# Kernel tuning notes

Hardware: AMD Instinct MI355X
Metric: run time of the kernel (lower is better)

Reference implementation:

```python
import jax, jax.numpy as jnp
import numpy as np
import math

N, IFZ, NVZ, AHZ, QPZ, KZ, PEZ = 1024, 256, 64, 8, 4, 20, 20
NUM_FREQ = PEZ // 2
FREQ_INV = 50.0

def layer_norm(x, g, b, eps=1e-5):
    mu = x.mean(-1, keepdims=True)
    var = ((x - mu) ** 2).mean(-1, keepdims=True)
    return (x - mu) / jnp.sqrt(var + eps) * g + b

def setup_inputs() -> dict:
    key = jax.random.key(0)
    ks = jax.random.split(key, 8)
    x = jax.random.normal(ks[0], (N, IFZ), jnp.float32)
    affines = jax.random.normal(ks[1], (N, 3, 4), jnp.float32)
    prot_mask = jnp.ones((N,), dtype=bool)
    edge_index = jax.random.randint(ks[2], (N, KZ), 0, N, dtype=jnp.int32)
    s = 0.02
    w_nde = jax.random.normal(ks[3], (KZ * 3 * PEZ, NVZ), jnp.float32) * s
    b_nde = jnp.zeros((NVZ,), jnp.float32)
    w_q = jax.random.normal(ks[4], (IFZ + NVZ, AHZ * QPZ * 3), jnp.float32) * s
    w_v = jax.random.normal(ks[5], (IFZ + NVZ, AHZ * QPZ * IFZ), jnp.float32) * s
    ln_ag_g = jnp.ones((AHZ * QPZ * IFZ,), jnp.float32)
    ln_ag_b = jnp.zeros((AHZ * QPZ * IFZ,), jnp.float32)
    w_ag = jax.random.normal(ks[6], (AHZ * QPZ * IFZ, IFZ), jnp.float32) * s
    ln_en_g = jnp.ones((IFZ,), jnp.float32)
    ln_en_b = jnp.zeros((IFZ,), jnp.float32)
    return dict(x=x, affines=affines, prot_mask=prot_mask, edge_index=edge_index,
                w_nde=w_nde, b_nde=b_nde, w_q=w_q, w_v=w_v,
                ln_ag_g=ln_ag_g, ln_ag_b=ln_ag_b, w_ag=w_ag,
                ln_en_g=ln_en_g, ln_en_b=ln_en_b)

def reference(x, affines, prot_mask, edge_index, w_nde, b_nde, w_q, w_v,
              ln_ag_g, ln_ag_b, w_ag, ln_en_g, ln_en_b):
    dtype = x.dtype
    R = affines[:, :, :3]                                   # (N,3,3) rotation
    t = affines[:, :, 3]                                    # (N,3) translation
    positions = t
    # --- BackboneDistanceEmbedding (reconstructed): local neighbour vectors ---
    rel = positions[edge_index] - t[:, None, :]             # (N,K,3)
    local = jnp.einsum('nji,nkj->nki', R, rel)              # inverse-affine (R^T) (N,K,3)
    freqs = jnp.arange(1, NUM_FREQ + 1, dtype=dtype) / FREQ_INV
    ang = local[..., None] * freqs                          # (N,K,3,F)
    pe = jnp.concatenate([jnp.sin(ang), jnp.cos(ang)], -1)  # (N,K,3,PEZ)
    nv = jax.nn.relu(pe.reshape(x.shape[0], -1) @ w_nde + b_nde)  # (N,NVZ)
    nv = nv * prot_mask[:, None].astype(dtype)
    x_ne = jnp.concatenate([x, nv], axis=-1)                # (N,IFZ+NVZ)
    # --- query points in global frame ---
    q = (x_ne @ w_q).reshape(-1, 1, AHZ, QPZ, 3)
    q = jnp.einsum('nij,nkaqj->nkaqi', R, q) + t[:, None, None, None, :]
    gnp = positions[edge_index][:, :, None, None, :]        # (N,K,1,1,3)
    # --- L2-distance attention over neighbourhood ---
    scores = -jnp.linalg.norm(q - gnp, axis=-1).sum(-1)     # (N,K,AHZ)
    attn = jax.nn.softmax(scores, axis=1).astype(dtype)
    # --- value gather + weighted aggregation ---
    v = (x_ne @ w_v).reshape(-1, AHZ, QPZ, IFZ)
    v_ne = v[edge_index]                                    # (N,K,AHZ,QPZ,IFZ) -- big gather
    new = jnp.einsum('nkaqi,nka->naqi', v_ne, attn).reshape(x.shape[0], -1)
    new = layer_norm(new, ln_ag_g, ln_ag_b) @ w_ag          # dropout: eval mode => identity
    out = layer_norm(x + new / math.sqrt(2.0), ln_en_g, ln_en_b).astype(dtype)
    return out, edge_index
```

## Files before the change

kernel.cpp:

```cpp
#include <hip/hip_runtime.h>
#include <hip/hip_bf16.h>
#include <math.h>

#define NNODE 1024
#define IFZ   256
#define NVZ   64
#define AHZ   8
#define QPZ   4
#define KZ    20
#define NF    10
#define XNE   320
#define VROW  8192
#define PEK   1280
#define PTOT  2560

typedef unsigned short ushort;
typedef __attribute__((ext_vector_type(8))) short    short8v;
typedef __attribute__((ext_vector_type(8))) ushort   ushort8v;
typedef __attribute__((ext_vector_type(4))) float    float4v;

static __device__ __forceinline__ ushort f2bf(float f) {
    unsigned u = __float_as_uint(f);
    unsigned r = 0x7FFFu + ((u >> 16) & 1u);
    return (ushort)((u + r) >> 16);
}
static __device__ __forceinline__ float bf2f(unsigned h) {
    return __uint_as_float(h << 16);
}

struct Params {
    const float *w_ag, *ln_ag_g, *ln_ag_b, *w_nde, *b_nde, *w_q, *w_v, *x, *aff;
    const int   *edge;
    const float *ln_en_g, *ln_en_b;
    ushort *wagT, *wndeT, *wqT, *wv_bf, *pebf, *xne_bf, *agg, *WcT, *G;
    float  *rsum, *vpart, *vconst, *qbuf, *geom, *S, *s2part, *tmpk, *out;
};

static __device__ __forceinline__ void gemm_tile(
    const ushort* __restrict__ A, const ushort* __restrict__ BT,
    int aStride, int btStride, int kLen, int bm, int bn, int tid,
    float4v acc[2][2], ushort (&As)[64][40], ushort (&Bs)[64][40])
{
    const int w = tid >> 6, lane = tid & 63;
    const int wr = w >> 1, wc = w & 1;
    const int lane15 = lane & 15, quad = lane >> 4;
    const int sm = tid >> 2, sk = (tid & 3) * 8;
    for (int k0 = 0; k0 < kLen; k0 += 32) {
        *(ushort8v*)&As[sm][sk] = *(const ushort8v*)&A[(size_t)(bm + sm)*aStride + k0 + sk];
        *(ushort8v*)&Bs[sm][sk] = *(const ushort8v*)&BT[(size_t)(bn + sm)*btStride + k0 + sk];
        __syncthreads();
        short8v a0 = *(const short8v*)&As[wr*32      + lane15][quad*8];
        short8v a1 = *(const short8v*)&As[wr*32 + 16 + lane15][quad*8];
        short8v b0 = *(const short8v*)&Bs[wc*32      + lane15][quad*8];
        short8v b1 = *(const short8v*)&Bs[wc*32 + 16 + lane15][quad*8];
        acc[0][0] = __builtin_amdgcn_mfma_f32_16x16x32_bf16(a0, b0, acc[0][0], 0, 0, 0);
        acc[0][1] = __builtin_amdgcn_mfma_f32_16x16x32_bf16(a0, b1, acc[0][1], 0, 0, 0);
        acc[1][0] = __builtin_amdgcn_mfma_f32_16x16x32_bf16(a1, b0, acc[1][0], 0, 0, 0);
        acc[1][1] = __builtin_amdgcn_mfma_f32_16x16x32_bf16(a1, b1, acc[1][1], 0, 0, 0);
        __syncthreads();
    }
}

#define T1_END 2048
#define T2_END 2128
#define T3_END 2168
#define CV_END 2488
#define GV_END 2552
#define K0_END 2808

__global__ __launch_bounds__(256) void k_prep(Params P)
{
    const int u = blockIdx.x;
    const int tid = threadIdx.x;
    __shared__ float t[32][33];
    __shared__ float part[256];
    __shared__ float tn[4][KZ][3];
    __shared__ float r9[4][9], tt[4][3];

    if (u < T3_END) {
        const float* src; ushort* dst; const float* scl;
        int R, C, gx, Rdst, rel;
        if (u < T1_END)      { src=P.w_ag; dst=P.wagT; scl=P.ln_ag_g; R=VROW; C=IFZ; gx=8; Rdst=VROW; rel=u; }
        else if (u < T2_END) { src=P.w_nde;dst=P.wndeT;scl=nullptr;   R=1200; C=NVZ; gx=2; Rdst=PEK;  rel=u-T1_END; }
        else                 { src=P.w_q;  dst=P.wqT;  scl=nullptr;   R=XNE;  C=96;  gx=4; Rdst=XNE;  rel=u-T2_END; }
        const int bx = rel % gx, by = rel / gx;
        const int c0 = bx*32, r0 = by*32;
        const int tx = tid & 31, ty = tid >> 5;
        #pragma unroll
        for (int i = 0; i < 4; ++i) {
            int r = r0 + ty + 8*i, c = c0 + tx;
            float v = (r < R && c < C) ? src[(size_t)r * C + c] : 0.f;
            if (scl && r < R) v *= scl[r];
            t[ty + 8*i][tx] = v;
        }
        __syncthreads();
        #pragma unroll
        for (int i = 0; i < 4; ++i)
            dst[(size_t)(c0 + ty + 8*i) * Rdst + r0 + tx] = f2bf(t[tx][ty + 8*i]);
    } else if (u < CV_END) {
        const int j = u - T3_END;
        const float* src = P.w_v + (size_t)j*VROW + tid*32;
        ushort* dst = P.wv_bf + (size_t)j*VROW + tid*32;
        float psum = 0.f;
        #pragma unroll
        for (int q = 0; q < 4; ++q) {
            float4 v0 = ((const float4*)src)[q*2];
            float4 v1 = ((const float4*)src)[q*2+1];
            psum += v0.x+v0.y+v0.z+v0.w + v1.x+v1.y+v1.z+v1.w;
            ushort8v o;
            o[0]=f2bf(v0.x); o[1]=f2bf(v0.y); o[2]=f2bf(v0.z); o[3]=f2bf(v0.w);
            o[4]=f2bf(v1.x); o[5]=f2bf(v1.y); o[6]=f2bf(v1.z); o[7]=f2bf(v1.w);
            *(ushort8v*)(dst + q*8) = o;
        }
        part[tid] = psum;
        __syncthreads();
        if (tid < 8) {
            float s = 0.f;
            #pragma unroll
            for (int v = 0; v < 32; ++v) s += part[tid*32 + v];
            P.rsum[tid*320 + j] = s;
        }
    } else if (u < GV_END) {
        const int sp = u - CV_END, j = tid;
        const float* base = P.w_ag + (size_t)sp * 128 * IFZ;
        float vp = 0.f, bp = 0.f;
        #pragma unroll 4
        for (int r = 0; r < 128; ++r) {
            float wv = base[(size_t)r * IFZ + j];
            vp += P.ln_ag_g[sp*128 + r] * wv;
            bp += P.ln_ag_b[sp*128 + r] * wv;
        }
        P.vpart[(size_t)(sp*2 + 0) * IFZ + j] = vp;
        P.vpart[(size_t)(sp*2 + 1) * IFZ + j] = bp;
    } else {
        const int rel = u - GV_END;
        const int wv = tid >> 6, lane = tid & 63;
        const int n = rel*4 + wv;
        if (lane < KZ) {
            int e = P.edge[n*KZ + lane];
            float a0 = P.aff[e*12 + 3], a1 = P.aff[e*12 + 7], a2 = P.aff[e*12 + 11];
            tn[wv][lane][0] = a0; tn[wv][lane][1] = a1; tn[wv][lane][2] = a2;
            P.geom[n*72 + 12 + lane*3 + 0] = a0;
            P.geom[n*72 + 12 + lane*3 + 1] = a1;
            P.geom[n*72 + 12 + lane*3 + 2] = a2;
        } else if (lane < 29) {
            int q = lane - 20;
            float v = P.aff[n*12 + (q/3)*4 + (q%3)];
            r9[wv][q] = v;
            P.geom[n*72 + q] = v;
        } else if (lane < 32) {
            float v = P.aff[n*12 + (lane-29)*4 + 3];
            tt[wv][lane-29] = v;
            P.geom[n*72 + 9 + (lane-29)] = v;
        }
        {
            float4 xv = ((const float4*)(P.x + (size_t)n*IFZ))[lane];
            unsigned lo = f2bf(xv.x) | ((unsigned)f2bf(xv.y) << 16);
            unsigned hi = f2bf(xv.z) | ((unsigned)f2bf(xv.w) << 16);
            unsigned* p = (unsigned*)(P.xne_bf + (size_t)n*XNE) + lane*2;
            p[0] = lo; p[1] = hi;
        }
        __syncthreads();
        if (lane < 60) {
            int k = lane / 3, i = lane % 3;
            float d0 = tn[wv][k][0]-tt[wv][0];
            float d1 = tn[wv][k][1]-tt[wv][1];
            float d2 = tn[wv][k][2]-tt[wv][2];
            float loc = r9[wv][0+i]*d0 + r9[wv][3+i]*d1 + r9[wv][6+i]*d2;
            size_t base = (size_t)n*PEK + k*60 + i*20;
            #pragma unroll
            for (int p = 0; p < NF; p += 2) {
                float a0 = loc * (float)(p+1) * (1.0f/50.0f);
                float a1 = loc * (float)(p+2) * (1.0f/50.0f);
                unsigned us = f2bf(__sinf(a0)) | ((unsigned)f2bf(__sinf(a1)) << 16);
                unsigned uc = f2bf(__cosf(a0)) | ((unsigned)f2bf(__cosf(a1)) << 16);
                *(unsigned*)&P.pebf[base + p]      = us;
                *(unsigned*)&P.pebf[base + 10 + p] = uc;
            }
        }
        if (lane < 40)
            *(unsigned*)&P.pebf[(size_t)n*PEK + 1200 + lane*2] = 0u;
    }
}

__global__ __launch_bounds__(256) void k_sjobs(Params P)
{
    const int u = blockIdx.x;
    const int tid = threadIdx.x;
    __shared__ ushort As[64][40];
    __shared__ ushort Bs[64][40];

    if (u >= 48) {
        int vb = u - 48;
        float s = 0.f;
        #pragma unroll 8
        for (int sp = 0; sp < 64; ++sp)
            s += P.vpart[(size_t)(sp*2 + vb)*IFZ + tid];
        P.vconst[vb*IFZ + tid] = s;
        return;
    }
    const ushort *A, *BT;
    int kLen, bm, bn, mode, aStr, btStr;
    if (u < 16) {
        A = P.pebf; BT = P.wndeT; aStr=PEK; btStr=PEK; kLen=PEK;
        bm = u*64; bn = 0; mode = 2;
    } else {
        int rel = u - 16; int bx = rel % 2, by = rel / 2;
        A = P.xne_bf; BT = P.wqT; aStr=XNE; btStr=XNE; kLen=256;
        bm = by*64; bn = bx*64; mode = 1;
    }
    float4v acc[2][2] = {};
    gemm_tile(A, BT, aStr, btStr, kLen, bm, bn, tid, acc, As, Bs);

    const int w = tid >> 6, lane = tid & 63;
    const int wr = w >> 1, wc = w & 1;
    const int lane15 = lane & 15, quad = lane >> 4;
    #pragma unroll
    for (int i = 0; i < 2; ++i) {
        #pragma unroll
        for (int j = 0; j < 2; ++j) {
            int col = bn + wc*32 + j*16 + lane15;
            #pragma unroll
            for (int r = 0; r < 4; ++r) {
                int row = bm + wr*32 + i*16 + quad*4 + r;
                float val = acc[i][j][r];
                if (mode == 2) {
                    val = fmaxf(val + P.b_nde[col], 0.f);
                    P.xne_bf[(size_t)row*XNE + IFZ + col] = f2bf(val);
                } else {
                    P.qbuf[(size_t)row*128 + col] = val;
                }
            }
        }
    }
}

union SharedM {
    struct { ushort As[64][40]; ushort Bs[64][40]; } g;
    struct { float geo[72], qf[96], qg[96], sc[160], at[160], nvr[64];
             float rs[PTOT], red[256]; int es[KZ]; ushort xs[KZ][XNE]; } s;
};

__global__ __launch_bounds__(256) void k_mid(Params P)
{
    const int u = blockIdx.x;
    const int tid = threadIdx.x;
    __shared__ SharedM sh;

    if (u < 360) {
        const ushort *A, *BT; ushort* Cb; size_t cbase; int bm, bn, ldc;
        if (u < 160) {
            int bx=u%5, by=(u/5)%4, bz=u/20;
            A = P.wagT + bz*1024; BT = P.wv_bf + bz*1024;
            bm=by*64; bn=bx*64; Cb=P.WcT; cbase=(size_t)bz*320; ldc=PTOT;
        } else {
            int rel=u-160; int bx=rel%5, by=(rel/5)%5, bz=rel/25;
            A = P.wv_bf + bz*1024; BT = P.wv_bf + bz*1024;
            bm=by*64; bn=bx*64; Cb=P.G; cbase=(size_t)bz*102400; ldc=320;
        }
        float4v acc[2][2] = {};
        gemm_tile(A, BT, VROW, VROW, 1024, bm, bn, tid, acc, sh.g.As, sh.g.Bs);

        const int w = tid >> 6, lane = tid & 63;
        const int wr = w >> 1, wc = w & 1;
        const int lane15 = lane & 15, quad = lane >> 4;
        #pragma unroll
        for (int i = 0; i < 2; ++i) {
            #pragma unroll
            for (int j = 0; j < 2; ++j) {
                int col = bn + wc*32 + j*16 + lane15;
                #pragma unroll
                for (int r = 0; r < 4; ++r) {
                    int row = bm + wr*32 + i*16 + quad*4 + r;
                    Cb[cbase + (size_t)row*ldc + col] = f2bf(acc[i][j][r]);
                }
            }
        }
        return;
    }

    const int n = u - 360;
    if (tid < 72) sh.s.geo[tid] = P.geom[n*72 + tid];
    if (tid < KZ) sh.s.es[tid] = P.edge[n*KZ + tid];
    if (tid < 64) sh.s.nvr[tid] = bf2f(P.xne_bf[(size_t)n*XNE + IFZ + tid]);
    for (int p = tid; p < PTOT; p += 256) sh.s.rs[p] = P.rsum[p];
    __syncthreads();

    for (int s = tid; s < KZ*40; s += 256) {
        int k = s / 40, ch = s % 40;
        *(ushort8v*)&sh.s.xs[k][ch*8] =
            *(const ushort8v*)&P.xne_bf[(size_t)sh.s.es[k]*XNE + ch*8];
    }
    if (tid < 96) {
        float qv = P.qbuf[n*128 + tid];
        #pragma unroll 16
        for (int r = 0; r < 64; ++r)
            qv += sh.s.nvr[r] * P.w_q[(256 + r)*96 + tid];
        sh.s.qf[tid] = qv;
    }
    __syncthreads();
    if (tid < 96) {
        int i = tid % 3, base = (tid/3)*3;
        sh.s.qg[tid] = sh.s.geo[i*3+0]*sh.s.qf[base] + sh.s.geo[i*3+1]*sh.s.qf[base+1]
                     + sh.s.geo[i*3+2]*sh.s.qf[base+2] + sh.s.geo[9+i];
    }
    __syncthreads();
    if (tid < 160) {
        int k = tid / 8, a = tid % 8;
        float tx = sh.s.geo[12+k*3+0], ty = sh.s.geo[12+k*3+1], tz = sh.s.geo[12+k*3+2];
        float acc = 0.f;
        #pragma unroll
        for (int qp = 0; qp < QPZ; ++qp) {
            int b = a*12 + qp*3;
            float dx = sh.s.qg[b]   - tx;
            float dy = sh.s.qg[b+1] - ty;
            float dz = sh.s.qg[b+2] - tz;
            acc += sqrtf(dx*dx + dy*dy + dz*dz);
        }
        sh.s.sc[a*20 + k] = -acc;
    }
    __syncthreads();
    if (tid < 8) {
        int a = tid;
        float m = -1e30f;
        #pragma unroll
        for (int k = 0; k < KZ; ++k) m = fmaxf(m, sh.s.sc[a*20+k]);
        float e[KZ]; float sum = 0.f;
        #pragma unroll
        for (int k = 0; k < KZ; ++k) { e[k] = __expf(sh.s.sc[a*20+k] - m); sum += e[k]; }
        float inv = 1.f / sum;
        #pragma unroll
        for (int k = 0; k < KZ; ++k) sh.s.at[k*8 + a] = e[k]*inv;
    }
    __syncthreads();

    float sp = 0.f;
    for (int s = tid; s < AHZ*40; s += 256) {
        int a = s / 40, ch = s % 40;
        float acc[8] = {};
        #pragma unroll 4
        for (int k = 0; k < KZ; ++k) {
            ushort8v p = *(const ushort8v*)&sh.s.xs[k][ch*8];
            float wgt = sh.s.at[k*8 + a];
            #pragma unroll
            for (int j = 0; j < 8; ++j)
                acc[j] += wgt * bf2f((ushort)p[j]);
        }
        ushort8v o;
        #pragma unroll
        for (int j = 0; j < 8; ++j) {
            o[j] = (short)f2bf(acc[j]);
            sp += acc[j] * sh.s.rs[a*320 + ch*8 + j];
        }
        *(ushort8v*)&P.agg[(size_t)n*PTOT + a*320 + ch*8] = o;
    }
    sh.s.red[tid] = sp;
    __syncthreads();
    if (tid < 64) {
        float v = sh.s.red[tid] + sh.s.red[tid+64] + sh.s.red[tid+128] + sh.s.red[tid+192];
        #pragma unroll
        for (int off = 32; off > 0; off >>= 1) v += __shfl_down(v, off, 64);
        if (tid == 0) P.S[n] = v;
    }
}

__global__ __launch_bounds__(256) void k_gemm_b(Params P)
{
    const int u = blockIdx.x;
    const int tid = threadIdx.x;
    __shared__ ushort As[64][40];
    __shared__ ushort Bs[64][40];
    const int w = tid >> 6, lane = tid & 63;
    const int wr = w >> 1, wc = w & 1;
    const int lane15 = lane & 15, quad = lane >> 4;
    float4v acc[2][2] = {};

    if (u < 640) {
        const int bx = u % 5, by = (u/5) % 16, a = u/80;
        const int bm = by*64, bn = bx*64;
        gemm_tile(P.agg + a*320, P.G + (size_t)a*102400,
                  PTOT, 320, 320, bm, bn, tid, acc, As, Bs);
        #pragma unroll
        for (int i = 0; i < 2; ++i) {
            #pragma unroll
            for (int r = 0; r < 4; ++r) {
                int row = bm + wr*32 + i*16 + quad*4 + r;
                int c0  = bn + wc*32 + lane15;
                float av0 = bf2f(P.agg[(size_t)row*PTOT + a*320 + c0]);
                float av1 = bf2f(P.agg[(size_t)row*PTOT + a*320 + c0 + 16]);
                float v = acc[i][0][r]*av0 + acc[i][1][r]*av1;
                v += __shfl_xor(v, 1, 64);
                v += __shfl_xor(v, 2, 64);
                v += __shfl_xor(v, 4, 64);
                v += __shfl_xor(v, 8, 64);
                if (lane15 == 0)
                    P.s2part[(size_t)row*80 + a*10 + (bn>>5) + wc] = v;
            }
        }
    } else {
        const int rel = u - 640;
        const int bx = rel % 4, by = (rel/4) % 16, z = rel/64;
        const int bm = by*64, bn = bx*64;
        gemm_tile(P.agg + z*1280, P.WcT + z*1280,
                  PTOT, PTOT, 1280, bm, bn, tid, acc, As, Bs);
        float* Cf = P.tmpk + (size_t)z*NNODE*IFZ;
        #pragma unroll
        for (int i = 0; i < 2; ++i) {
            #pragma unroll
            for (int j = 0; j < 2; ++j) {
                int col = bn + wc*32 + j*16 + lane15;
                #pragma unroll
                for (int r = 0; r < 4; ++r) {
                    int row = bm + wr*32 + i*16 + quad*4 + r;
                    Cf[(size_t)row*IFZ + col] = acc[i][j][r];
                }
            }
        }
    }
}

__global__ __launch_bounds__(256) void k_final(Params P)
{
    const int n = blockIdx.x;
    const int tid = threadIdx.x;
    __shared__ float wsum[4], wsq[4];
    __shared__ float s_mu8, s_rstd8, s_mu, s_rstd;
    const int wid = tid >> 6, lane = tid & 63;

    float v = (tid < 80) ? P.s2part[(size_t)n*80 + tid] : 0.f;
    #pragma unroll
    for (int off = 32; off > 0; off >>= 1) v += __shfl_down(v, off, 64);
    if (lane == 0) wsum[wid] = v;
    __syncthreads();
    if (tid == 0) {
        float S2 = wsum[0]+wsum[1]+wsum[2]+wsum[3];
        float Sv = P.S[n];
        float mu = Sv * (1.f/(float)VROW);
        float var = S2 * (1.f/(float)VROW) - mu*mu;
        s_mu8 = mu; s_rstd8 = rsqrtf(var + 1e-5f);
    }
    __syncthreads();
    const float mu8 = s_mu8, rstd8 = s_rstd8;

    float s = P.tmpk[n*IFZ + tid] + P.tmpk[NNODE*IFZ + n*IFZ + tid];
    float vc = P.vconst[tid], bc = P.vconst[IFZ + tid];
    float pre = rstd8*s - rstd8*mu8*vc + bc;

    float val = P.x[n*IFZ + tid] + pre * 0.70710678118654752f;
    float lsum = val, lsq = val*val;
    #pragma unroll
    for (int off = 32; off > 0; off >>= 1) {
        lsum += __shfl_down(lsum, off, 64);
        lsq  += __shfl_down(lsq,  off, 64);
    }
    __syncthreads();
    if (lane == 0) { wsum[wid] = lsum; wsq[wid] = lsq; }
    __syncthreads();
    if (tid == 0) {
        float ts = wsum[0]+wsum[1]+wsum[2]+wsum[3];
        float tq = wsq[0]+wsq[1]+wsq[2]+wsq[3];
        float mu = ts / (float)IFZ;
        float var = tq / (float)IFZ - mu*mu;
        s_mu = mu; s_rstd = rsqrtf(var + 1e-5f);
    }
    __syncthreads();
    P.out[n*IFZ + tid] = (val - s_mu)*s_rstd*P.ln_en_g[tid] + P.ln_en_b[tid];
    if (tid < KZ)
        P.out[NNODE*IFZ + n*KZ + tid] = (float)P.edge[n*KZ + tid];
}

extern "C" void kernel_launch(void* const* d_in, const int* in_sizes, int n_in,
                              void* d_out, int out_size, void* d_ws, size_t ws_size,
                              hipStream_t stream)
{
    char* w = (char*)d_ws;
    Params P;
    P.x       = (const float*)d_in[0];
    P.aff     = (const float*)d_in[1];
    P.edge    = (const int*)d_in[3];
    P.w_nde   = (const float*)d_in[4];
    P.b_nde   = (const float*)d_in[5];
    P.w_q     = (const float*)d_in[6];
    P.w_v     = (const float*)d_in[7];
    P.ln_ag_g = (const float*)d_in[8];
    P.ln_ag_b = (const float*)d_in[9];
    P.w_ag    = (const float*)d_in[10];
    P.ln_en_g = (const float*)d_in[11];
    P.ln_en_b = (const float*)d_in[12];
    P.out     = (float*)d_out;

    P.xne_bf = (ushort*)(w + 0x0);
    P.qbuf   = (float*) (w + 0xA0000);
    P.vpart  = (float*) (w + 0x120000);
    P.vconst = (float*) (w + 0x140000);
    P.wagT   = (ushort*)(w + 0x250000);
    P.wv_bf  = (ushort*)(w + 0x650000);
    P.WcT    = (ushort*)(w + 0xB50000);
    P.G      = (ushort*)(w + 0xC90000);
    P.rsum   = (float*) (w + 0xE20000);
    P.S      = (float*) (w + 0xE23000);
    P.s2part = (float*) (w + 0xE24000);
    P.agg    = (ushort*)(w + 0xE80000);
    P.tmpk   = (float*) (w + 0x1380000);
    P.pebf   = (ushort*)(w + 0x1580000);
    P.wndeT  = (ushort*)(w + 0x1800000);
    P.wqT    = (ushort*)(w + 0x1828000);
    P.geom   = (float*) (w + 0x1840000);

    hipLaunchKernelGGL(k_prep,   dim3(K0_END), dim3(256), 0, stream, P);
    hipLaunchKernelGGL(k_sjobs,  dim3(50),     dim3(256), 0, stream, P);
    hipLaunchKernelGGL(k_mid,    dim3(1384),   dim3(256), 0, stream, P);
    hipLaunchKernelGGL(k_gemm_b, dim3(768),    dim3(256), 0, stream, P);
    hipLaunchKernelGGL(k_final,  dim3(NNODE),  dim3(256), 0, stream, P);
}
```

Baseline: 170.8 us.

## Rebalance weight-prep jobs into the small-GEMM launch to fill idle CUs

Moves the large weight conversion, w_ag transpose and LN-fold partial-sum jobs out of the first kernel into the second kernel alongside the 48 small GEMM tiles. The vconst reduction moves into the mid kernel. This shortens the critical path, since the small GEMMs no longer wait behind thousands of independent prep blocks and the GPU is no longer underused during the tiny launch. It relies on the job dependencies staying satisfied across launches and adds some shared-memory union complexity.

```diff
diff --git a/kernel.cpp b/kernel.cpp
--- a/kernel.cpp
+++ b/kernel.cpp
@@ -61,81 +61,21 @@
     }
 }
 
-#define T1_END 2048
-#define T2_END 2128
-#define T3_END 2168
-#define CV_END 2488
-#define GV_END 2552
-#define K0_END 2808
+#define PA_K0  256
+#define PA_T2  336
+#define PA_T3  376
 
 __global__ __launch_bounds__(256) void k_prep(Params P)
 {
     const int u = blockIdx.x;
     const int tid = threadIdx.x;
     __shared__ float t[32][33];
-    __shared__ float part[256];
     __shared__ float tn[4][KZ][3];
     __shared__ float r9[4][9], tt[4][3];
 
-    if (u < T3_END) {
-        const float* src; ushort* dst; const float* scl;
-        int R, C, gx, Rdst, rel;
-        if (u < T1_END)      { src=P.w_ag; dst=P.wagT; scl=P.ln_ag_g; R=VROW; C=IFZ; gx=8; Rdst=VROW; rel=u; }
-        else if (u < T2_END) { src=P.w_nde;dst=P.wndeT;scl=nullptr;   R=1200; C=NVZ; gx=2; Rdst=PEK;  rel=u-T1_END; }
-        else                 { src=P.w_q;  dst=P.wqT;  scl=nullptr;   R=XNE;  C=96;  gx=4; Rdst=XNE;  rel=u-T2_END; }
-        const int bx = rel % gx, by = rel / gx;
-        const int c0 = bx*32, r0 = by*32;
-        const int tx = tid & 31, ty = tid >> 5;
-        #pragma unroll
-        for (int i = 0; i < 4; ++i) {
-            int r = r0 + ty + 8*i, c = c0 + tx;
-            float v = (r < R && c < C) ? src[(size_t)r * C + c] : 0.f;
-            if (scl && r < R) v *= scl[r];
-            t[ty + 8*i][tx] = v;
-        }
-        __syncthreads();
-        #pragma unroll
-        for (int i = 0; i < 4; ++i)
-            dst[(size_t)(c0 + ty + 8*i) * Rdst + r0 + tx] = f2bf(t[tx][ty + 8*i]);
-    } else if (u < CV_END) {
-        const int j = u - T3_END;
-        const float* src = P.w_v + (size_t)j*VROW + tid*32;
-        ushort* dst = P.wv_bf + (size_t)j*VROW + tid*32;
-        float psum = 0.f;
-        #pragma unroll
-        for (int q = 0; q < 4; ++q) {
-            float4 v0 = ((const float4*)src)[q*2];
-            float4 v1 = ((const float4*)src)[q*2+1];
-            psum += v0.x+v0.y+v0.z+v0.w + v1.x+v1.y+v1.z+v1.w;
-            ushort8v o;
-            o[0]=f2bf(v0.x); o[1]=f2bf(v0.y); o[2]=f2bf(v0.z); o[3]=f2bf(v0.w);
-            o[4]=f2bf(v1.x); o[5]=f2bf(v1.y); o[6]=f2bf(v1.z); o[7]=f2bf(v1.w);
-            *(ushort8v*)(dst + q*8) = o;
-        }
-        part[tid] = psum;
-        __syncthreads();
-        if (tid < 8) {
-            float s = 0.f;
-            #pragma unroll
-            for (int v = 0; v < 32; ++v) s += part[tid*32 + v];
-            P.rsum[tid*320 + j] = s;
-        }
-    } else if (u < GV_END) {
-        const int sp = u - CV_END, j = tid;
-        const float* base = P.w_ag + (size_t)sp * 128 * IFZ;
-        float vp = 0.f, bp = 0.f;
-        #pragma unroll 4
-        for (int r = 0; r < 128; ++r) {
-            float wv = base[(size_t)r * IFZ + j];
-            vp += P.ln_ag_g[sp*128 + r] * wv;
-            bp += P.ln_ag_b[sp*128 + r] * wv;
-        }
-        P.vpart[(size_t)(sp*2 + 0) * IFZ + j] = vp;
-        P.vpart[(size_t)(sp*2 + 1) * IFZ + j] = bp;
-    } else {
-        const int rel = u - GV_END;
+    if (u < PA_K0) {
         const int wv = tid >> 6, lane = tid & 63;
-        const int n = rel*4 + wv;
+        const int n = u*4 + wv;
         if (lane < KZ) {
             int e = P.edge[n*KZ + lane];
             float a0 = P.aff[e*12 + 3], a1 = P.aff[e*12 + 7], a2 = P.aff[e*12 + 11];
@@ -180,58 +120,128 @@
         }
         if (lane < 40)
             *(unsigned*)&P.pebf[(size_t)n*PEK + 1200 + lane*2] = 0u;
-    }
-}
-
-__global__ __launch_bounds__(256) void k_sjobs(Params P)
+    } else {
+        const float* src; ushort* dst;
+        int R, C, gx, Rdst, rel;
+        if (u < PA_T2) { src=P.w_nde; dst=P.wndeT; R=1200; C=NVZ; gx=2; Rdst=PEK; rel=u-PA_K0; }
+        else           { src=P.w_q;   dst=P.wqT;   R=XNE;  C=96;  gx=4; Rdst=XNE; rel=u-PA_T2; }
+        const int bx = rel % gx, by = rel / gx;
+        const int c0 = bx*32, r0 = by*32;
+        const int tx = tid & 31, ty = tid >> 5;
+        #pragma unroll
+        for (int i = 0; i < 4; ++i) {
+            int r = r0 + ty + 8*i, c = c0 + tx;
+            t[ty + 8*i][tx] = (r < R && c < C) ? src[(size_t)r * C + c] : 0.f;
+        }
+        __syncthreads();
+        #pragma unroll
+        for (int i = 0; i < 4; ++i)
+            dst[(size_t)(c0 + ty + 8*i) * Rdst + r0 + tx] = f2bf(t[tx][ty + 8*i]);
+    }
+}
+
+#define WJ_NV  16
+#define WJ_QX  48
+#define WJ_CV  368
+#define WJ_T1  2416
+#define WJ_GV  2480
+
+union SharedW {
+    struct { ushort As[64][40]; ushort Bs[64][40]; } g;
+    struct { float t[32][33]; } t1;
+    struct { float part[256]; } cv;
+};
+
+__global__ __launch_bounds__(256) void k_wjobs(Params P)
 {
     const int u = blockIdx.x;
     const int tid = threadIdx.x;
-    __shared__ ushort As[64][40];
-    __shared__ ushort Bs[64][40];
-
-    if (u >= 48) {
-        int vb = u - 48;
-        float s = 0.f;
-        #pragma unroll 8
-        for (int sp = 0; sp < 64; ++sp)
-            s += P.vpart[(size_t)(sp*2 + vb)*IFZ + tid];
-        P.vconst[vb*IFZ + tid] = s;
-        return;
-    }
-    const ushort *A, *BT;
-    int kLen, bm, bn, mode, aStr, btStr;
-    if (u < 16) {
-        A = P.pebf; BT = P.wndeT; aStr=PEK; btStr=PEK; kLen=PEK;
-        bm = u*64; bn = 0; mode = 2;
-    } else {
-        int rel = u - 16; int bx = rel % 2, by = rel / 2;
-        A = P.xne_bf; BT = P.wqT; aStr=XNE; btStr=XNE; kLen=256;
-        bm = by*64; bn = bx*64; mode = 1;
-    }
-    float4v acc[2][2] = {};
-    gemm_tile(A, BT, aStr, btStr, kLen, bm, bn, tid, acc, As, Bs);
-
-    const int w = tid >> 6, lane = tid & 63;
-    const int wr = w >> 1, wc = w & 1;
-    const int lane15 = lane & 15, quad = lane >> 4;
-    #pragma unroll
-    for (int i = 0; i < 2; ++i) {
-        #pragma unroll
-        for (int j = 0; j < 2; ++j) {
-            int col = bn + wc*32 + j*16 + lane15;
-            #pragma unroll
-            for (int r = 0; r < 4; ++r) {
-                int row = bm + wr*32 + i*16 + quad*4 + r;
-                float val = acc[i][j][r];
-                if (mode == 2) {
-                    val = fmaxf(val + P.b_nde[col], 0.f);
-                    P.xne_bf[(size_t)row*XNE + IFZ + col] = f2bf(val);
-                } else {
-                    P.qbuf[(size_t)row*128 + col] = val;
+    __shared__ SharedW sh;
+
+    if (u < WJ_QX) {
+        const ushort *A, *BT;
+        int kLen, bm, bn, mode, aStr, btStr;
+        if (u < WJ_NV) {
+            A = P.pebf; BT = P.wndeT; aStr=PEK; btStr=PEK; kLen=PEK;
+            bm = u*64; bn = 0; mode = 2;
+        } else {
+            int rel = u - WJ_NV; int bx = rel % 2, by = rel / 2;
+            A = P.xne_bf; BT = P.wqT; aStr=XNE; btStr=XNE; kLen=256;
+            bm = by*64; bn = bx*64; mode = 1;
+        }
+        float4v acc[2][2] = {};
+        gemm_tile(A, BT, aStr, btStr, kLen, bm, bn, tid, acc, sh.g.As, sh.g.Bs);
+
+        const int w = tid >> 6, lane = tid & 63;
+        const int wr = w >> 1, wc = w & 1;
+        const int lane15 = lane & 15, quad = lane >> 4;
+        #pragma unroll
+        for (int i = 0; i < 2; ++i) {
+            #pragma unroll
+            for (int j = 0; j < 2; ++j) {
+                int col = bn + wc*32 + j*16 + lane15;
+                #pragma unroll
+                for (int r = 0; r < 4; ++r) {
+                    int row = bm + wr*32 + i*16 + quad*4 + r;
+                    float val = acc[i][j][r];
+                    if (mode == 2) {
+                        val = fmaxf(val + P.b_nde[col], 0.f);
+                        P.xne_bf[(size_t)row*XNE + IFZ + col] = f2bf(val);
+                    } else {
+                        P.qbuf[(size_t)row*128 + col] = val;
+                    }
                 }
             }
         }
+    } else if (u < WJ_CV) {
+        const int j = u - WJ_QX;
+        const float* src = P.w_v + (size_t)j*VROW + tid*32;
+        ushort* dst = P.wv_bf + (size_t)j*VROW + tid*32;
+        float psum = 0.f;
+        #pragma unroll
+        for (int q = 0; q < 4; ++q) {
+            float4 v0 = ((const float4*)src)[q*2];
+            float4 v1 = ((const float4*)src)[q*2+1];
+            psum += v0.x+v0.y+v0.z+v0.w + v1.x+v1.y+v1.z+v1.w;
+            ushort8v o;
+            o[0]=f2bf(v0.x); o[1]=f2bf(v0.y); o[2]=f2bf(v0.z); o[3]=f2bf(v0.w);
+            o[4]=f2bf(v1.x); o[5]=f2bf(v1.y); o[6]=f2bf(v1.z); o[7]=f2bf(v1.w);
+            *(ushort8v*)(dst + q*8) = o;
+        }
+        sh.cv.part[tid] = psum;
+        __syncthreads();
+        if (tid < 8) {
+            float s = 0.f;
+            #pragma unroll
+            for (int v = 0; v < 32; ++v) s += sh.cv.part[tid*32 + v];
+            P.rsum[tid*320 + j] = s;
+        }
+    } else if (u < WJ_T1) {
+        const int rel = u - WJ_CV;
+        const int bx = rel % 8, by = rel / 8;
+        const int c0 = bx*32, r0 = by*32;
+        const int tx = tid & 31, ty = tid >> 5;
+        #pragma unroll
+        for (int i = 0; i < 4; ++i) {
+            int r = r0 + ty + 8*i, c = c0 + tx;
+            sh.t1.t[ty + 8*i][tx] = P.w_ag[(size_t)r * IFZ + c] * P.ln_ag_g[r];
+        }
+        __syncthreads();
+        #pragma unroll
+        for (int i = 0; i < 4; ++i)
+            P.wagT[(size_t)(c0 + ty + 8*i) * VROW + r0 + tx] = f2bf(sh.t1.t[tx][ty + 8*i]);
+    } else {
+        const int sp = u - WJ_T1, j = tid;
+        const float* base = P.w_ag + (size_t)sp * 128 * IFZ;
+        float vp = 0.f, bp = 0.f;
+        #pragma unroll 4
+        for (int r = 0; r < 128; ++r) {
+            float wv = base[(size_t)r * IFZ + j];
+            vp += P.ln_ag_g[sp*128 + r] * wv;
+            bp += P.ln_ag_b[sp*128 + r] * wv;
+        }
+        P.vpart[(size_t)(sp*2 + 0) * IFZ + j] = vp;
+        P.vpart[(size_t)(sp*2 + 1) * IFZ + j] = bp;
     }
 }
 
@@ -278,8 +288,17 @@
         }
         return;
     }
-
-    const int n = u - 360;
+    if (u < 362) {
+        int vb = u - 360;
+        float s = 0.f;
+        #pragma unroll 8
+        for (int sp = 0; sp < 64; ++sp)
+            s += P.vpart[(size_t)(sp*2 + vb)*IFZ + tid];
+        P.vconst[vb*IFZ + tid] = s;
+        return;
+    }
+
+    const int n = u - 362;
     if (tid < 72) sh.s.geo[tid] = P.geom[n*72 + tid];
     if (tid < KZ) sh.s.es[tid] = P.edge[n*KZ + tid];
     if (tid < 64) sh.s.nvr[tid] = bf2f(P.xne_bf[(size_t)n*XNE + IFZ + tid]);
@@ -507,9 +526,9 @@
     P.wqT    = (ushort*)(w + 0x1828000);
     P.geom   = (float*) (w + 0x1840000);
 
-    hipLaunchKernelGGL(k_prep,   dim3(K0_END), dim3(256), 0, stream, P);
-    hipLaunchKernelGGL(k_sjobs,  dim3(50),     dim3(256), 0, stream, P);
-    hipLaunchKernelGGL(k_mid,    dim3(1384),   dim3(256), 0, stream, P);
+    hipLaunchKernelGGL(k_prep,   dim3(PA_T3),  dim3(256), 0, stream, P);
+    hipLaunchKernelGGL(k_wjobs,  dim3(WJ_GV),  dim3(256), 0, stream, P);
+    hipLaunchKernelGGL(k_mid,    dim3(1386),   dim3(256), 0, stream, P);
     hipLaunchKernelGGL(k_gemm_b, dim3(768),    dim3(256), 0, stream, P);
     hipLaunchKernelGGL(k_final,  dim3(NNODE),  dim3(256), 0, stream, P);
 }
```

Result: faster. 161.1 us (-5.7%).
